# Performance work log

Measured on AMD Instinct MI355X. Metric: run time of the kernel, lower is better.

The kernel has to match this reference:

```python
import jax, jax.numpy as jnp
import numpy as np

IN_FEATURES = 4096
OUT_FEATURES = 16384
B, S = 8, 16  # small token count -> weight-traffic bound (decode-like)


def setup_inputs() -> dict:
    key = jax.random.key(0)
    k_x, k_w, k_b = jax.random.split(key, 3)
    x = jax.random.normal(k_x, (B, S, IN_FEATURES), dtype=jnp.float32)
    # symmetric int8 quantized weight, values in [-127, 127]
    weight_int = jax.random.randint(k_w, (OUT_FEATURES, IN_FEATURES), -127, 128, dtype=jnp.int32)
    weight_scale = jnp.float32(0.01)      # scalar scale (symmetric, per-tensor)
    weight_zero_point = jnp.float32(0.0)  # symmetric -> zero_point = 0
    bias = jax.random.normal(k_b, (OUT_FEATURES,), dtype=jnp.float32)
    return {"x": x, "weight_int": weight_int, "weight_scale": weight_scale,
            "weight_zero_point": weight_zero_point, "bias": bias}


def reference(x, weight_int, weight_scale, weight_zero_point, bias):
    # dequantize: (q - zp) * scale, then F.linear: x @ W^T + b
    weight_float = (weight_int.astype(jnp.float32) - weight_zero_point) * weight_scale
    # x: [B, S, in], weight_float: [out, in] -> [B, S, out]
    return jnp.einsum('bsi,oi->bso', x, weight_float) + bias
```

## Files before the change

### kernel.cpp

```cpp
#include <hip/hip_runtime.h>
#include <hip/hip_bf16.h>


#define IN_F 4096
#define OUT_F 16384
#define NTOK 128

typedef __attribute__((ext_vector_type(8))) short bf16x8;
typedef __attribute__((ext_vector_type(4))) float f32x4;

__device__ __forceinline__ unsigned short f32_to_bf16_rne(float f) {
  unsigned u = __float_as_uint(f);
  u += 0x7fffu + ((u >> 16) & 1u);
  return (unsigned short)(u >> 16);
}

__global__ __launch_bounds__(512) void prep_x(const float* __restrict__ x,
                                              uint4* __restrict__ xf,
                                              float* __restrict__ xsum) {
  const int token = blockIdx.x;
  const int i = (int)threadIdx.x;
  const int k0 = i << 3;
  const float4 v0 = *(const float4*)(x + token * IN_F + k0);
  const float4 v1 = *(const float4*)(x + token * IN_F + k0 + 4);
  float v[8] = {v0.x, v0.y, v0.z, v0.w, v1.x, v1.y, v1.z, v1.w};
  unsigned short h[8];
  float s = 0.f;
#pragma unroll
  for (int j = 0; j < 8; ++j) {
    s += v[j];
    h[j] = f32_to_bf16_rne(v[j]);
  }
  uint4 o;
  o.x = (unsigned)h[0] | ((unsigned)h[1] << 16);
  o.y = (unsigned)h[2] | ((unsigned)h[3] << 16);
  o.z = (unsigned)h[4] | ((unsigned)h[5] << 16);
  o.w = (unsigned)h[6] | ((unsigned)h[7] << 16);
  const int slab = i >> 2;
  const int q = i & 3;
  const int lane = (q << 4) | (token & 15);
  xf[slab * 512 + (token >> 4) * 64 + lane] = o;

#pragma unroll
  for (int off = 32; off > 0; off >>= 1) s += __shfl_down(s, off, 64);
  __shared__ float wsum[8];
  if ((i & 63) == 0) wsum[i >> 6] = s;
  __syncthreads();
  if (i == 0) {
    float t = 0.f;
#pragma unroll
    for (int a = 0; a < 8; ++a) t += wsum[a];
    xsum[token] = t;
  }
}

__device__ __forceinline__ bf16x8 cvt8(int4 a, int4 b) {
  bf16x8 o;
  o[0] = (short)(__float_as_uint((float)a.x) >> 16);
  o[1] = (short)(__float_as_uint((float)a.y) >> 16);
  o[2] = (short)(__float_as_uint((float)a.z) >> 16);
  o[3] = (short)(__float_as_uint((float)a.w) >> 16);
  o[4] = (short)(__float_as_uint((float)b.x) >> 16);
  o[5] = (short)(__float_as_uint((float)b.y) >> 16);
  o[6] = (short)(__float_as_uint((float)b.z) >> 16);
  o[7] = (short)(__float_as_uint((float)b.w) >> 16);
  return o;
}

__global__ __launch_bounds__(256, 2) void qlinear_main(
    const int* __restrict__ W, const uint4* __restrict__ xf,
    const float* __restrict__ xsum, const float* __restrict__ scale_p,
    const float* __restrict__ zp_p, const float* __restrict__ bias,
    float* __restrict__ out) {
  __shared__ int smem[16384];

  const int tid = (int)threadIdx.x;
  const int w = tid >> 6;
  const int l = tid & 63;
  const int q = l >> 4;
  const int r = l & 15;
  const int R0 = (int)blockIdx.x * 32;

  const int row_l = l >> 3;
  const int col_l = (l & 7) * 4;
  const int* Wl = W + (R0 + row_l) * IN_F + w * 1024 + col_l;
  const uint4* xp = xf + (w * 32) * 512 + l;

  int* const sw = smem + w * 2048;
  int* const sdl = sw + row_l * 32 + col_l;
  const int* const srl0 = sw + r * 32 + q * 8;
  const int* const srl1 = sw + (16 + r) * 32 + q * 8;

  f32x4 acc[2][8];
#pragma unroll
  for (int n = 0; n < 2; ++n)
#pragma unroll
    for (int t = 0; t < 8; ++t) acc[n][t] = (f32x4)0.0f;

  const int kk0 = ((int)blockIdx.x * 7) & 31;

  uint4 B0[8], B1[8];
  int4 G0, G1, G2, G3;

  {
    const int kk = kk0;
    G0 = *(const int4*)(Wl + kk * 32);
    G1 = *(const int4*)(Wl + 8 * IN_F + kk * 32);
    G2 = *(const int4*)(Wl + 16 * IN_F + kk * 32);
    G3 = *(const int4*)(Wl + 24 * IN_F + kk * 32);
#pragma unroll
    for (int t = 0; t < 8; ++t) B0[t] = xp[kk * 512 + t * 64];
    *(int4*)(sdl + 0) = G0;
    *(int4*)(sdl + 256) = G1;
    *(int4*)(sdl + 512) = G2;
    *(int4*)(sdl + 768) = G3;
  }

  for (int it = 0; it < 16; ++it) {
    const int i2 = it * 2;
    const int kkB = (kk0 + i2 + 1) & 31;
    const int kkC = (kk0 + i2 + 2) & 31;

    G0 = *(const int4*)(Wl + kkB * 32);
    G1 = *(const int4*)(Wl + 8 * IN_F + kkB * 32);
    G2 = *(const int4*)(Wl + 16 * IN_F + kkB * 32);
    G3 = *(const int4*)(Wl + 24 * IN_F + kkB * 32);
#pragma unroll
    for (int t = 0; t < 8; ++t) B1[t] = xp[kkB * 512 + t * 64];

    {
      int4 x0 = *(const int4*)(srl0);
      int4 x1 = *(const int4*)(srl0 + 4);
      int4 y0 = *(const int4*)(srl1);
      int4 y1 = *(const int4*)(srl1 + 4);
      bf16x8 a0 = cvt8(x0, x1);
      bf16x8 a1 = cvt8(y0, y1);
#pragma unroll
      for (int t = 0; t < 8; ++t) {
        bf16x8 bf = *(const bf16x8*)&B0[t];
        acc[0][t] = __builtin_amdgcn_mfma_f32_16x16x32_bf16(a0, bf, acc[0][t], 0, 0, 0);
        acc[1][t] = __builtin_amdgcn_mfma_f32_16x16x32_bf16(a1, bf, acc[1][t], 0, 0, 0);
      }
    }
    *(int4*)(sdl + 1024) = G0;
    *(int4*)(sdl + 1024 + 256) = G1;
    *(int4*)(sdl + 1024 + 512) = G2;
    *(int4*)(sdl + 1024 + 768) = G3;

    if (it != 15) {
      G0 = *(const int4*)(Wl + kkC * 32);
      G1 = *(const int4*)(Wl + 8 * IN_F + kkC * 32);
      G2 = *(const int4*)(Wl + 16 * IN_F + kkC * 32);
      G3 = *(const int4*)(Wl + 24 * IN_F + kkC * 32);
#pragma unroll
      for (int t = 0; t < 8; ++t) B0[t] = xp[kkC * 512 + t * 64];
    }

    {
      int4 x0 = *(const int4*)(srl0 + 1024);
      int4 x1 = *(const int4*)(srl0 + 1024 + 4);
      int4 y0 = *(const int4*)(srl1 + 1024);
      int4 y1 = *(const int4*)(srl1 + 1024 + 4);
      bf16x8 a0 = cvt8(x0, x1);
      bf16x8 a1 = cvt8(y0, y1);
#pragma unroll
      for (int t = 0; t < 8; ++t) {
        bf16x8 bf = *(const bf16x8*)&B1[t];
        acc[0][t] = __builtin_amdgcn_mfma_f32_16x16x32_bf16(a0, bf, acc[0][t], 0, 0, 0);
        acc[1][t] = __builtin_amdgcn_mfma_f32_16x16x32_bf16(a1, bf, acc[1][t], 0, 0, 0);
      }
    }
    if (it != 15) {
      *(int4*)(sdl + 0) = G0;
      *(int4*)(sdl + 256) = G1;
      *(int4*)(sdl + 512) = G2;
      *(int4*)(sdl + 768) = G3;
    }
  }

  __syncthreads();
  {
    float* sp = (float*)smem;
#pragma unroll
    for (int n = 0; n < 2; ++n)
#pragma unroll
      for (int t = 0; t < 8; ++t)
        *(f32x4*)(sp + w * 4096 + (n * 8 + t) * 256 + l * 4) = acc[n][t];
  }
  __syncthreads();
  const float scale = *scale_p;
  const float zp = *zp_p;
  const float czp = scale * zp;
  const float* sp = (const float*)smem;
#pragma unroll
  for (int j = 0; j < 4; ++j) {
    const int c = w * 4 + j;
    const int n = c >> 3;
    const int t = c & 7;
    f32x4 s0 = *(const f32x4*)(sp + 0 * 4096 + c * 256 + l * 4);
    f32x4 s1 = *(const f32x4*)(sp + 1 * 4096 + c * 256 + l * 4);
    f32x4 s2 = *(const f32x4*)(sp + 2 * 4096 + c * 256 + l * 4);
    f32x4 s3 = *(const f32x4*)(sp + 3 * 4096 + c * 256 + l * 4);
    f32x4 s = (s0 + s1) + (s2 + s3);
    const int token = t * 16 + r;
    const float corr = -czp * xsum[token];
    const int feat = R0 + n * 16 + q * 4;
    const float4 bv = *(const float4*)(bias + feat);
    float4 o;
    o.x = s[0] * scale + corr + bv.x;
    o.y = s[1] * scale + corr + bv.y;
    o.z = s[2] * scale + corr + bv.z;
    o.w = s[3] * scale + corr + bv.w;
    *(float4*)(out + token * OUT_F + feat) = o;
  }
}

extern "C" void kernel_launch(void* const* d_in, const int* in_sizes, int n_in,
                              void* d_out, int out_size, void* d_ws, size_t ws_size,
                              hipStream_t stream) {
  const float* x = (const float*)d_in[0];
  const int* W = (const int*)d_in[1];
  const float* scale = (const float*)d_in[2];
  const float* zp = (const float*)d_in[3];
  const float* bias = (const float*)d_in[4];
  float* out = (float*)d_out;

  uint4* xf = (uint4*)d_ws;
  float* xsum = (float*)((char*)d_ws + (1 << 20));

  prep_x<<<NTOK, 512, 0, stream>>>(x, xf, xsum);
  qlinear_main<<<OUT_F / 32, 256, 0, stream>>>(W, xf, xsum, scale, zp, bias, out);
}
```

Before: 378.8 us.

## Split tokens across waves and share bf16 weight tiles via LDS

The main kernel now runs 512 threads per block. Each of the 8 waves owns one 16-token group and walks the full K dimension, instead of each wave owning a K quarter and reducing partial sums through LDS at the end. Weights are converted to bf16 once, when they are written to a padded, double-buffered LDS tile shared by all waves, which removes the per-wave conversion and the final cross-wave reduction. The cost is two block barriers per K step, and each wave reloads the activation fragments.

```diff
diff --git a/kernel.cpp b/kernel.cpp
--- a/kernel.cpp
+++ b/kernel.cpp
@@ -54,25 +54,23 @@
   }
 }
 
-__device__ __forceinline__ bf16x8 cvt8(int4 a, int4 b) {
-  bf16x8 o;
-  o[0] = (short)(__float_as_uint((float)a.x) >> 16);
-  o[1] = (short)(__float_as_uint((float)a.y) >> 16);
-  o[2] = (short)(__float_as_uint((float)a.z) >> 16);
-  o[3] = (short)(__float_as_uint((float)a.w) >> 16);
-  o[4] = (short)(__float_as_uint((float)b.x) >> 16);
-  o[5] = (short)(__float_as_uint((float)b.y) >> 16);
-  o[6] = (short)(__float_as_uint((float)b.z) >> 16);
-  o[7] = (short)(__float_as_uint((float)b.w) >> 16);
-  return o;
-}
-
-__global__ __launch_bounds__(256, 2) void qlinear_main(
+__device__ __forceinline__ void stash4(short* lds_s, int off_s, int4 v) {
+  uint2 o;
+  o.x = (__float_as_uint((float)v.x) >> 16) | (__float_as_uint((float)v.y) & 0xffff0000u);
+  o.y = (__float_as_uint((float)v.z) >> 16) | (__float_as_uint((float)v.w) & 0xffff0000u);
+  *(uint2*)(lds_s + off_s) = o;
+}
+
+#define SROW 40
+#define SSL 1280
+#define SBUF 5120
+
+__global__ __launch_bounds__(512, 4) void qlinear_main(
     const int* __restrict__ W, const uint4* __restrict__ xf,
     const float* __restrict__ xsum, const float* __restrict__ scale_p,
     const float* __restrict__ zp_p, const float* __restrict__ bias,
     float* __restrict__ out) {
-  __shared__ int smem[16384];
+  __shared__ short smem[2 * SBUF];
 
   const int tid = (int)threadIdx.x;
   const int w = tid >> 6;
@@ -81,137 +79,108 @@
   const int r = l & 15;
   const int R0 = (int)blockIdx.x * 32;
 
-  const int row_l = l >> 3;
-  const int col_l = (l & 7) * 4;
-  const int* Wl = W + (R0 + row_l) * IN_F + w * 1024 + col_l;
-  const uint4* xp = xf + (w * 32) * 512 + l;
-
-  int* const sw = smem + w * 2048;
-  int* const sdl = sw + row_l * 32 + col_l;
-  const int* const srl0 = sw + r * 32 + q * 8;
-  const int* const srl1 = sw + (16 + r) * 32 + q * 8;
-
-  f32x4 acc[2][8];
-#pragma unroll
-  for (int n = 0; n < 2; ++n)
-#pragma unroll
-    for (int t = 0; t < 8; ++t) acc[n][t] = (f32x4)0.0f;
-
-  const int kk0 = ((int)blockIdx.x * 7) & 31;
-
-  uint4 B0[8], B1[8];
-  int4 G0, G1, G2, G3;
+  const int row0 = tid >> 5;
+  const int c0 = (tid & 31) * 4;
+  const int sl = c0 >> 5;
+  const int kk = c0 & 31;
+  const int g0 = (R0 + row0) * IN_F + c0;
+  const int g1 = (R0 + row0 + 16) * IN_F + c0;
+  const int w0 = sl * SSL + row0 * SROW + kk;
+  const int w1 = sl * SSL + (row0 + 16) * SROW + kk;
+
+  const int a0off = r * SROW + q * 8;
+  const int a1off = (16 + r) * SROW + q * 8;
+
+  const uint4* xp = xf + w * 64 + l;
+
+  f32x4 acc0 = (f32x4)0.0f, acc1 = (f32x4)0.0f;
+
+  const int p0 = ((int)blockIdx.x * 13) & 31;
+
+  int4 WnA, WnB;
+  int4 WfA, WfB;
+  uint4 Bc[4], Bn[4];
 
   {
-    const int kk = kk0;
-    G0 = *(const int4*)(Wl + kk * 32);
-    G1 = *(const int4*)(Wl + 8 * IN_F + kk * 32);
-    G2 = *(const int4*)(Wl + 16 * IN_F + kk * 32);
-    G3 = *(const int4*)(Wl + 24 * IN_F + kk * 32);
-#pragma unroll
-    for (int t = 0; t < 8; ++t) B0[t] = xp[kk * 512 + t * 64];
-    *(int4*)(sdl + 0) = G0;
-    *(int4*)(sdl + 256) = G1;
-    *(int4*)(sdl + 512) = G2;
-    *(int4*)(sdl + 768) = G3;
-  }
-
+    const int ppk = p0 * 128;
+    int4 t0 = *(const int4*)(W + g0 + ppk);
+    int4 t1 = *(const int4*)(W + g1 + ppk);
+#pragma unroll
+    for (int s = 0; s < 4; ++s) Bc[s] = xp[(p0 * 4 + s) * 512];
+    const int pp1k = (((p0 + 1) & 31) * 128);
+    WnA = *(const int4*)(W + g0 + pp1k);
+    WnB = *(const int4*)(W + g1 + pp1k);
+    stash4(smem, w0, t0);
+    stash4(smem, w1, t1);
+  }
+  __syncthreads();
+
+#pragma unroll 1
   for (int it = 0; it < 16; ++it) {
-    const int i2 = it * 2;
-    const int kkB = (kk0 + i2 + 1) & 31;
-    const int kkC = (kk0 + i2 + 2) & 31;
-
-    G0 = *(const int4*)(Wl + kkB * 32);
-    G1 = *(const int4*)(Wl + 8 * IN_F + kkB * 32);
-    G2 = *(const int4*)(Wl + 16 * IN_F + kkB * 32);
-    G3 = *(const int4*)(Wl + 24 * IN_F + kkB * 32);
-#pragma unroll
-    for (int t = 0; t < 8; ++t) B1[t] = xp[kkB * 512 + t * 64];
-
     {
-      int4 x0 = *(const int4*)(srl0);
-      int4 x1 = *(const int4*)(srl0 + 4);
-      int4 y0 = *(const int4*)(srl1);
-      int4 y1 = *(const int4*)(srl1 + 4);
-      bf16x8 a0 = cvt8(x0, x1);
-      bf16x8 a1 = cvt8(y0, y1);
-#pragma unroll
-      for (int t = 0; t < 8; ++t) {
-        bf16x8 bf = *(const bf16x8*)&B0[t];
-        acc[0][t] = __builtin_amdgcn_mfma_f32_16x16x32_bf16(a0, bf, acc[0][t], 0, 0, 0);
-        acc[1][t] = __builtin_amdgcn_mfma_f32_16x16x32_bf16(a1, bf, acc[1][t], 0, 0, 0);
+      const int ppf = ((2 * it + 2 + p0) & 31) * 128;
+      WfA = *(const int4*)(W + g0 + ppf);
+      WfB = *(const int4*)(W + g1 + ppf);
+      const int ppb = (2 * it + 1 + p0) & 31;
+#pragma unroll
+      for (int s = 0; s < 4; ++s) Bn[s] = xp[(ppb * 4 + s) * 512];
+#pragma unroll
+      for (int s = 0; s < 4; ++s) {
+        bf16x8 a0 = *(const bf16x8*)(smem + s * SSL + a0off);
+        bf16x8 a1 = *(const bf16x8*)(smem + s * SSL + a1off);
+        bf16x8 b = *(const bf16x8*)&Bc[s];
+        acc0 = __builtin_amdgcn_mfma_f32_16x16x32_bf16(a0, b, acc0, 0, 0, 0);
+        acc1 = __builtin_amdgcn_mfma_f32_16x16x32_bf16(a1, b, acc1, 0, 0, 0);
       }
+      __syncthreads();
+      stash4(smem + SBUF, w0, WnA);
+      stash4(smem + SBUF, w1, WnB);
+      __syncthreads();
     }
-    *(int4*)(sdl + 1024) = G0;
-    *(int4*)(sdl + 1024 + 256) = G1;
-    *(int4*)(sdl + 1024 + 512) = G2;
-    *(int4*)(sdl + 1024 + 768) = G3;
-
-    if (it != 15) {
-      G0 = *(const int4*)(Wl + kkC * 32);
-      G1 = *(const int4*)(Wl + 8 * IN_F + kkC * 32);
-      G2 = *(const int4*)(Wl + 16 * IN_F + kkC * 32);
-      G3 = *(const int4*)(Wl + 24 * IN_F + kkC * 32);
-#pragma unroll
-      for (int t = 0; t < 8; ++t) B0[t] = xp[kkC * 512 + t * 64];
+    {
+      const int ppf = ((2 * it + 3 + p0) & 31) * 128;
+      WnA = *(const int4*)(W + g0 + ppf);
+      WnB = *(const int4*)(W + g1 + ppf);
+      const int ppb = (2 * it + 2 + p0) & 31;
+#pragma unroll
+      for (int s = 0; s < 4; ++s) Bc[s] = xp[(ppb * 4 + s) * 512];
+#pragma unroll
+      for (int s = 0; s < 4; ++s) {
+        bf16x8 a0 = *(const bf16x8*)(smem + SBUF + s * SSL + a0off);
+        bf16x8 a1 = *(const bf16x8*)(smem + SBUF + s * SSL + a1off);
+        bf16x8 b = *(const bf16x8*)&Bn[s];
+        acc0 = __builtin_amdgcn_mfma_f32_16x16x32_bf16(a0, b, acc0, 0, 0, 0);
+        acc1 = __builtin_amdgcn_mfma_f32_16x16x32_bf16(a1, b, acc1, 0, 0, 0);
+      }
+      __syncthreads();
+      stash4(smem, w0, WfA);
+      stash4(smem, w1, WfB);
+      __syncthreads();
     }
-
-    {
-      int4 x0 = *(const int4*)(srl0 + 1024);
-      int4 x1 = *(const int4*)(srl0 + 1024 + 4);
-      int4 y0 = *(const int4*)(srl1 + 1024);
-      int4 y1 = *(const int4*)(srl1 + 1024 + 4);
-      bf16x8 a0 = cvt8(x0, x1);
-      bf16x8 a1 = cvt8(y0, y1);
-#pragma unroll
-      for (int t = 0; t < 8; ++t) {
-        bf16x8 bf = *(const bf16x8*)&B1[t];
-        acc[0][t] = __builtin_amdgcn_mfma_f32_16x16x32_bf16(a0, bf, acc[0][t], 0, 0, 0);
-        acc[1][t] = __builtin_amdgcn_mfma_f32_16x16x32_bf16(a1, bf, acc[1][t], 0, 0, 0);
-      }
-    }
-    if (it != 15) {
-      *(int4*)(sdl + 0) = G0;
-      *(int4*)(sdl + 256) = G1;
-      *(int4*)(sdl + 512) = G2;
-      *(int4*)(sdl + 768) = G3;
-    }
-  }
-
-  __syncthreads();
-  {
-    float* sp = (float*)smem;
-#pragma unroll
-    for (int n = 0; n < 2; ++n)
-#pragma unroll
-      for (int t = 0; t < 8; ++t)
-        *(f32x4*)(sp + w * 4096 + (n * 8 + t) * 256 + l * 4) = acc[n][t];
-  }
-  __syncthreads();
+  }
+
   const float scale = *scale_p;
   const float zp = *zp_p;
-  const float czp = scale * zp;
-  const float* sp = (const float*)smem;
-#pragma unroll
-  for (int j = 0; j < 4; ++j) {
-    const int c = w * 4 + j;
-    const int n = c >> 3;
-    const int t = c & 7;
-    f32x4 s0 = *(const f32x4*)(sp + 0 * 4096 + c * 256 + l * 4);
-    f32x4 s1 = *(const f32x4*)(sp + 1 * 4096 + c * 256 + l * 4);
-    f32x4 s2 = *(const f32x4*)(sp + 2 * 4096 + c * 256 + l * 4);
-    f32x4 s3 = *(const f32x4*)(sp + 3 * 4096 + c * 256 + l * 4);
-    f32x4 s = (s0 + s1) + (s2 + s3);
-    const int token = t * 16 + r;
-    const float corr = -czp * xsum[token];
-    const int feat = R0 + n * 16 + q * 4;
-    const float4 bv = *(const float4*)(bias + feat);
+  const int token = w * 16 + r;
+  const float corr = -scale * zp * xsum[token];
+  float* orow = out + token * OUT_F + R0 + q * 4;
+  {
+    const float4 bv = *(const float4*)(bias + R0 + q * 4);
     float4 o;
-    o.x = s[0] * scale + corr + bv.x;
-    o.y = s[1] * scale + corr + bv.y;
-    o.z = s[2] * scale + corr + bv.z;
-    o.w = s[3] * scale + corr + bv.w;
-    *(float4*)(out + token * OUT_F + feat) = o;
+    o.x = acc0[0] * scale + corr + bv.x;
+    o.y = acc0[1] * scale + corr + bv.y;
+    o.z = acc0[2] * scale + corr + bv.z;
+    o.w = acc0[3] * scale + corr + bv.w;
+    *(float4*)(orow) = o;
+  }
+  {
+    const float4 bv = *(const float4*)(bias + R0 + 16 + q * 4);
+    float4 o;
+    o.x = acc1[0] * scale + corr + bv.x;
+    o.y = acc1[1] * scale + corr + bv.y;
+    o.z = acc1[2] * scale + corr + bv.z;
+    o.w = acc1[3] * scale + corr + bv.w;
+    *(float4*)(orow + 16) = o;
   }
 }
 
@@ -229,5 +198,5 @@
   float* xsum = (float*)((char*)d_ws + (1 << 20));
 
   prep_x<<<NTOK, 512, 0, stream>>>(x, xf, xsum);
-  qlinear_main<<<OUT_F / 32, 256, 0, stream>>>(W, xf, xsum, scale, zp, bias, out);
-}
+  qlinear_main<<<OUT_F / 32, 512, 0, stream>>>(W, xf, xsum, scale, zp, bias, out);
+}
```

New measurement: 370.3 us. -2.3%, faster.

## Restructure GEMV into single-wave blocks with register-only deep prefetch, no LDS

Applied to the files above, without the earlier changes.

Replaces the 4-wave block that staged int32 weights through shared memory and split K across waves with a single 64-lane wave per 16-row tile. That wave covers the full K range, loading weights straight from global into registers in the MFMA A-fragment layout, with an 8-deep weight prefetch and a 2-deep activation prefetch. This removes the LDS round trips, the cross-wave reduction and the barriers, and doubles the grid size. In exchange each wave re-reads the whole activation buffer from global/L2 for every 16 rows, and the weight row loads are strided, which may reduce coalescing and raise register pressure.

```diff
diff --git a/kernel.cpp b/kernel.cpp
--- a/kernel.cpp
+++ b/kernel.cpp
@@ -67,151 +67,107 @@
   return o;
 }
 
-__global__ __launch_bounds__(256, 2) void qlinear_main(
+__global__ __launch_bounds__(64, 1) void qlinear_main(
     const int* __restrict__ W, const uint4* __restrict__ xf,
     const float* __restrict__ xsum, const float* __restrict__ scale_p,
     const float* __restrict__ zp_p, const float* __restrict__ bias,
     float* __restrict__ out) {
-  __shared__ int smem[16384];
-
-  const int tid = (int)threadIdx.x;
-  const int w = tid >> 6;
-  const int l = tid & 63;
+  const int l = (int)threadIdx.x;
   const int q = l >> 4;
   const int r = l & 15;
-  const int R0 = (int)blockIdx.x * 32;
+  const int rt = (int)blockIdx.x;
+  const int R0 = rt * 16;
 
-  const int row_l = l >> 3;
-  const int col_l = (l & 7) * 4;
-  const int* Wl = W + (R0 + row_l) * IN_F + w * 1024 + col_l;
-  const uint4* xp = xf + (w * 32) * 512 + l;
+  const int* Wbase = W + (R0 + r) * IN_F + q * 8;
+  const int start = (rt * 37) & 127;
 
-  int* const sw = smem + w * 2048;
-  int* const sdl = sw + row_l * 32 + col_l;
-  const int* const srl0 = sw + r * 32 + q * 8;
-  const int* const srl1 = sw + (16 + r) * 32 + q * 8;
+  int4 wa[8], wb[8];
+  uint4 bb[2][8];
 
-  f32x4 acc[2][8];
+  f32x4 acc[8];
 #pragma unroll
-  for (int n = 0; n < 2; ++n)
+  for (int t = 0; t < 8; ++t) acc[t] = (f32x4)0.0f;
+
 #pragma unroll
-    for (int t = 0; t < 8; ++t) acc[n][t] = (f32x4)0.0f;
-
-  const int kk0 = ((int)blockIdx.x * 7) & 31;
-
-  uint4 B0[8], B1[8];
-  int4 G0, G1, G2, G3;
-
-  {
-    const int kk = kk0;
-    G0 = *(const int4*)(Wl + kk * 32);
-    G1 = *(const int4*)(Wl + 8 * IN_F + kk * 32);
-    G2 = *(const int4*)(Wl + 16 * IN_F + kk * 32);
-    G3 = *(const int4*)(Wl + 24 * IN_F + kk * 32);
+  for (int d = 0; d < 8; ++d) {
+    const int kk = (start + d) & 127;
+    wa[d] = *(const int4*)(Wbase + kk * 32);
+    wb[d] = *(const int4*)(Wbase + kk * 32 + 4);
+  }
 #pragma unroll
-    for (int t = 0; t < 8; ++t) B0[t] = xp[kk * 512 + t * 64];
-    *(int4*)(sdl + 0) = G0;
-    *(int4*)(sdl + 256) = G1;
-    *(int4*)(sdl + 512) = G2;
-    *(int4*)(sdl + 768) = G3;
+  for (int d = 0; d < 2; ++d) {
+    const int kk = (start + d) & 127;
+    const uint4* xp = xf + kk * 512 + l;
+#pragma unroll
+    for (int t = 0; t < 8; ++t) bb[d][t] = xp[t * 64];
   }
 
-  for (int it = 0; it < 16; ++it) {
-    const int i2 = it * 2;
-    const int kkB = (kk0 + i2 + 1) & 31;
-    const int kkC = (kk0 + i2 + 2) & 31;
-
-    G0 = *(const int4*)(Wl + kkB * 32);
-    G1 = *(const int4*)(Wl + 8 * IN_F + kkB * 32);
-    G2 = *(const int4*)(Wl + 16 * IN_F + kkB * 32);
-    G3 = *(const int4*)(Wl + 24 * IN_F + kkB * 32);
+#pragma unroll 1
+  for (int k = 0; k <= 112; k += 8) {
 #pragma unroll
-    for (int t = 0; t < 8; ++t) B1[t] = xp[kkB * 512 + t * 64];
-
-    {
-      int4 x0 = *(const int4*)(srl0);
-      int4 x1 = *(const int4*)(srl0 + 4);
-      int4 y0 = *(const int4*)(srl1);
-      int4 y1 = *(const int4*)(srl1 + 4);
-      bf16x8 a0 = cvt8(x0, x1);
-      bf16x8 a1 = cvt8(y0, y1);
+    for (int u = 0; u < 8; ++u) {
+      const int step = k + u;
+      {
+        const int kk = (start + step + 2) & 127;
+        const uint4* xp = xf + kk * 512 + l;
+        uint4 nb0 = xp[0 * 64], nb1 = xp[1 * 64], nb2 = xp[2 * 64], nb3 = xp[3 * 64];
+        uint4 nb4 = xp[4 * 64], nb5 = xp[5 * 64], nb6 = xp[6 * 64], nb7 = xp[7 * 64];
+        const int kw = (start + step + 8) & 127;
+        int4 nwa = *(const int4*)(Wbase + kw * 32);
+        int4 nwb = *(const int4*)(Wbase + kw * 32 + 4);
+        bf16x8 a = cvt8(wa[u], wb[u]);
+        wa[u] = nwa;
+        wb[u] = nwb;
+#pragma unroll
+        for (int t = 0; t < 8; ++t) {
+          bf16x8 b = *(const bf16x8*)&bb[u & 1][t];
+          acc[t] = __builtin_amdgcn_mfma_f32_16x16x32_bf16(a, b, acc[t], 0, 0, 0);
+        }
+        bb[u & 1][0] = nb0; bb[u & 1][1] = nb1; bb[u & 1][2] = nb2; bb[u & 1][3] = nb3;
+        bb[u & 1][4] = nb4; bb[u & 1][5] = nb5; bb[u & 1][6] = nb6; bb[u & 1][7] = nb7;
+      }
+    }
+  }
+#pragma unroll
+  for (int u = 0; u < 8; ++u) {
+    const int step = 120 + u;
+    bf16x8 a = cvt8(wa[u], wb[u]);
+    if (u < 6) {
+      const int kk = (start + step + 2) & 127;
+      const uint4* xp = xf + kk * 512 + l;
+      uint4 nb[8];
+#pragma unroll
+      for (int t = 0; t < 8; ++t) nb[t] = xp[t * 64];
 #pragma unroll
       for (int t = 0; t < 8; ++t) {
-        bf16x8 bf = *(const bf16x8*)&B0[t];
-        acc[0][t] = __builtin_amdgcn_mfma_f32_16x16x32_bf16(a0, bf, acc[0][t], 0, 0, 0);
-        acc[1][t] = __builtin_amdgcn_mfma_f32_16x16x32_bf16(a1, bf, acc[1][t], 0, 0, 0);
+        bf16x8 b = *(const bf16x8*)&bb[u & 1][t];
+        acc[t] = __builtin_amdgcn_mfma_f32_16x16x32_bf16(a, b, acc[t], 0, 0, 0);
       }
-    }
-    *(int4*)(sdl + 1024) = G0;
-    *(int4*)(sdl + 1024 + 256) = G1;
-    *(int4*)(sdl + 1024 + 512) = G2;
-    *(int4*)(sdl + 1024 + 768) = G3;
-
-    if (it != 15) {
-      G0 = *(const int4*)(Wl + kkC * 32);
-      G1 = *(const int4*)(Wl + 8 * IN_F + kkC * 32);
-      G2 = *(const int4*)(Wl + 16 * IN_F + kkC * 32);
-      G3 = *(const int4*)(Wl + 24 * IN_F + kkC * 32);
 #pragma unroll
-      for (int t = 0; t < 8; ++t) B0[t] = xp[kkC * 512 + t * 64];
-    }
-
-    {
-      int4 x0 = *(const int4*)(srl0 + 1024);
-      int4 x1 = *(const int4*)(srl0 + 1024 + 4);
-      int4 y0 = *(const int4*)(srl1 + 1024);
-      int4 y1 = *(const int4*)(srl1 + 1024 + 4);
-      bf16x8 a0 = cvt8(x0, x1);
-      bf16x8 a1 = cvt8(y0, y1);
+      for (int t = 0; t < 8; ++t) bb[u & 1][t] = nb[t];
+    } else {
 #pragma unroll
       for (int t = 0; t < 8; ++t) {
-        bf16x8 bf = *(const bf16x8*)&B1[t];
-        acc[0][t] = __builtin_amdgcn_mfma_f32_16x16x32_bf16(a0, bf, acc[0][t], 0, 0, 0);
-        acc[1][t] = __builtin_amdgcn_mfma_f32_16x16x32_bf16(a1, bf, acc[1][t], 0, 0, 0);
+        bf16x8 b = *(const bf16x8*)&bb[u & 1][t];
+        acc[t] = __builtin_amdgcn_mfma_f32_16x16x32_bf16(a, b, acc[t], 0, 0, 0);
       }
-    }
-    if (it != 15) {
-      *(int4*)(sdl + 0) = G0;
-      *(int4*)(sdl + 256) = G1;
-      *(int4*)(sdl + 512) = G2;
-      *(int4*)(sdl + 768) = G3;
     }
   }
 
-  __syncthreads();
-  {
-    float* sp = (float*)smem;
-#pragma unroll
-    for (int n = 0; n < 2; ++n)
-#pragma unroll
-      for (int t = 0; t < 8; ++t)
-        *(f32x4*)(sp + w * 4096 + (n * 8 + t) * 256 + l * 4) = acc[n][t];
-  }
-  __syncthreads();
   const float scale = *scale_p;
   const float zp = *zp_p;
   const float czp = scale * zp;
-  const float* sp = (const float*)smem;
+  const float4 bv = *(const float4*)(bias + R0 + q * 4);
 #pragma unroll
-  for (int j = 0; j < 4; ++j) {
-    const int c = w * 4 + j;
-    const int n = c >> 3;
-    const int t = c & 7;
-    f32x4 s0 = *(const f32x4*)(sp + 0 * 4096 + c * 256 + l * 4);
-    f32x4 s1 = *(const f32x4*)(sp + 1 * 4096 + c * 256 + l * 4);
-    f32x4 s2 = *(const f32x4*)(sp + 2 * 4096 + c * 256 + l * 4);
-    f32x4 s3 = *(const f32x4*)(sp + 3 * 4096 + c * 256 + l * 4);
-    f32x4 s = (s0 + s1) + (s2 + s3);
+  for (int t = 0; t < 8; ++t) {
     const int token = t * 16 + r;
     const float corr = -czp * xsum[token];
-    const int feat = R0 + n * 16 + q * 4;
-    const float4 bv = *(const float4*)(bias + feat);
     float4 o;
-    o.x = s[0] * scale + corr + bv.x;
-    o.y = s[1] * scale + corr + bv.y;
-    o.z = s[2] * scale + corr + bv.z;
-    o.w = s[3] * scale + corr + bv.w;
-    *(float4*)(out + token * OUT_F + feat) = o;
+    o.x = acc[t][0] * scale + corr + bv.x;
+    o.y = acc[t][1] * scale + corr + bv.y;
+    o.z = acc[t][2] * scale + corr + bv.z;
+    o.w = acc[t][3] * scale + corr + bv.w;
+    *(float4*)(out + token * OUT_F + R0 + q * 4) = o;
   }
 }
 
@@ -229,5 +185,5 @@
   float* xsum = (float*)((char*)d_ws + (1 << 20));
 
   prep_x<<<NTOK, 512, 0, stream>>>(x, xf, xsum);
-  qlinear_main<<<OUT_F / 32, 256, 0, stream>>>(W, xf, xsum, scale, zp, bias, out);
+  qlinear_main<<<OUT_F / 16, 64, 0, stream>>>(W, xf, xsum, scale, zp, bias, out);
 }
```

After: 401.7 us. +6.0%, slower.
